# Kernel tuning notes

Hardware: AMD Instinct MI355X
Metric: run time of the kernel (lower is better)

The kernel has to match this reference:

```python
import jax, jax.numpy as jnp
import numpy as np

DIM = 1024
HEADS = 16
HEAD_DIM = DIM // HEADS
SCALE = HEAD_DIM ** -0.5


def setup_inputs() -> dict:
    key = jax.random.key(0)
    ks = jax.random.split(key, 9)
    b, n, m = 4, 1024, 1024
    x = jax.random.normal(ks[0], (b, n, DIM), dtype=jnp.float32)
    context = jax.random.normal(ks[1], (b, m, DIM), dtype=jnp.float32)
    mask = jax.random.randint(ks[2], (b, n, 32, 32), 0, 2, dtype=jnp.int32)
    s = DIM ** -0.5
    Wq = jax.random.normal(ks[3], (DIM, DIM), dtype=jnp.float32) * s
    bq = jnp.zeros((DIM,), dtype=jnp.float32)
    Wkv = jax.random.normal(ks[4], (DIM, 2 * DIM), dtype=jnp.float32) * s
    bkv = jnp.zeros((2 * DIM,), dtype=jnp.float32)
    Wp = jax.random.normal(ks[5], (DIM, DIM), dtype=jnp.float32) * s
    bp = jnp.zeros((DIM,), dtype=jnp.float32)
    return {"x": x, "context": context, "mask": mask,
            "Wq": Wq, "bq": bq, "Wkv": Wkv, "bkv": bkv, "Wp": Wp, "bp": bp}


def reference(x, context, mask, Wq, bq, Wkv, bkv, Wp, bp):
    b, n, _ = x.shape
    m = context.shape[1]
    h, d = HEADS, HEAD_DIM
    # projections
    q = (x @ Wq + bq).reshape(b, n, h, d).transpose(0, 2, 1, 3)       # [b,h,n,d]
    kv = (context @ Wkv + bkv).reshape(b, m, 2, h, d)
    k = kv[:, :, 0].transpose(0, 2, 1, 3)                              # [b,h,m,d]
    v = kv[:, :, 1].transpose(0, 2, 1, 3)                              # [b,h,m,d]
    dots = jnp.einsum('bhnd,bhmd->bhnm', q, k) * SCALE                 # [b,h,n,m]
    # mask: [b,n,H,W] -> [b,1,n,m]; masked_fill where mask == 0
    mflat = mask.reshape(b, n, m)[:, None]                             # [b,1,n,m]
    dots = jnp.where(mflat == 0, -jnp.inf, dots)
    attn = jax.nn.softmax(dots, axis=-1)
    out = jnp.einsum('bhnm,bhmd->bhnd', attn, v)
    out = out.transpose(0, 2, 1, 3).reshape(b, n, h * d)
    return out @ Wp + bp
```

## Files before the change

### kernel.cpp

```cpp
#include <hip/hip_runtime.h>

typedef __bf16 bf16;
typedef __bf16 bf16x8 __attribute__((ext_vector_type(8)));
typedef float f32x4 __attribute__((ext_vector_type(4)));
typedef unsigned long long u64;

#define MFMA16(a, b, c) __builtin_amdgcn_mfma_f32_16x16x32_bf16(a, b, c, 0, 0, 0)

__device__ __forceinline__ void gl_lds16(const void* g, void* l) {
  __builtin_amdgcn_global_load_lds(
      (const __attribute__((address_space(1))) unsigned int*)g,
      (__attribute__((address_space(3))) unsigned int*)l, 16, 0, 0);
}

__global__ __launch_bounds__(256)
void prep_k(const float* __restrict__ Wq, const float* __restrict__ Wkv,
            const float* __restrict__ Wp, const int* __restrict__ mask,
            const float* __restrict__ context, const float* __restrict__ x,
            bf16* __restrict__ BqkvT, bf16* __restrict__ WpT,
            u64* __restrict__ maskbits, bf16* __restrict__ cb,
            bf16* __restrict__ xb) {
  const int bx = blockIdx.x;
  const int tid = threadIdx.x;
  if (bx >= 3328) {
    const size_t i = ((size_t)(bx - 3328) * 256 + tid) * 8;
    f32x4 a0 = *(const f32x4*)(x + i);
    f32x4 a1 = *(const f32x4*)(x + i + 4);
    bf16x8 t;
#pragma unroll
    for (int j = 0; j < 4; ++j) { t[j] = (bf16)a0[j]; t[4 + j] = (bf16)a1[j]; }
    *(bf16x8*)(xb + i) = t;
    return;
  }
  if (bx >= 1280) {
    const size_t i = ((size_t)(bx - 1280) * 256 + tid) * 8;
    f32x4 a0 = *(const f32x4*)(context + i);
    f32x4 a1 = *(const f32x4*)(context + i + 4);
    bf16x8 t;
#pragma unroll
    for (int j = 0; j < 4; ++j) { t[j] = (bf16)a0[j]; t[4 + j] = (bf16)a1[j]; }
    *(bf16x8*)(cb + i) = t;
    return;
  }
  if (bx >= 1024) {
    const int idx = (bx - 1024) * 256 + tid;
    const int4* p = (const int4*)(mask + (size_t)idx * 64);
    u64 v = 0;
#pragma unroll
    for (int i = 0; i < 16; ++i) {
      int4 m = p[i];
      v |= (u64)(m.x != 0) << (4 * i);
      v |= (u64)(m.y != 0) << (4 * i + 1);
      v |= (u64)(m.z != 0) << (4 * i + 2);
      v |= (u64)(m.w != 0) << (4 * i + 3);
    }
    maskbits[idx] = v;
    return;
  }
  const int ct = bx >> 4, rt = bx & 15;
  const float* src;
  bf16* dst;
  int C, c0, drow0;
  if (ct < 16) {
    src = Wq; C = 1024; c0 = ct * 64; dst = BqkvT; drow0 = c0;
  } else if (ct < 48) {
    src = Wkv; C = 2048; c0 = (ct - 16) * 64; dst = BqkvT; drow0 = 1024 + c0;
  } else {
    src = Wp; C = 1024; c0 = (ct - 48) * 64; dst = WpT; drow0 = c0;
  }
  __shared__ bf16 T[64][72];
  const int r0 = rt * 64;
#pragma unroll
  for (int i = 0; i < 2; ++i) {
    int c = i * 256 + tid;
    int row = c >> 3, col = (c & 7) * 8;
    const float* sp = &src[(size_t)(r0 + row) * C + c0 + col];
    f32x4 a0 = *(const f32x4*)sp;
    f32x4 a1 = *(const f32x4*)(sp + 4);
    bf16x8 t;
#pragma unroll
    for (int j = 0; j < 4; ++j) { t[j] = (bf16)a0[j]; t[4 + j] = (bf16)a1[j]; }
    *(bf16x8*)&T[row][col] = t;
  }
  __syncthreads();
#pragma unroll
  for (int i = 0; i < 2; ++i) {
    int c = i * 256 + tid;
    int orow = c >> 3, ocol = (c & 7) * 8;
    bf16x8 v;
#pragma unroll
    for (int j = 0; j < 8; ++j) v[j] = T[ocol + j][orow];
    *(bf16x8*)&dst[(size_t)(drow0 + orow) * 1024 + r0 + ocol] = v;
  }
}

template <int EPI, int BN>
__global__ __launch_bounds__(256)
void gemm_sb(const bf16* __restrict__ A0, const bf16* __restrict__ A1,
             const bf16* __restrict__ Bt, const float* __restrict__ bias0,
             const float* __restrict__ bias1, bf16* __restrict__ oq,
             bf16* __restrict__ ok, bf16* __restrict__ ovt,
             float* __restrict__ outf) {
  constexpr int NJ = BN / 32;
  __shared__ bf16 As[128][64];
  __shared__ bf16 Bs[BN][64];
  const int tid = threadIdx.x;
  const int lane = tid & 63;
  const int w = tid >> 6;
  const int wm = (w >> 1) * 64;
  const int wn = (w & 1) * (BN / 2);
  const int l15 = lane & 15, l4 = lane >> 4;
  const int lrow = lane >> 3;
  const int scol = ((lane & 7) ^ (lrow & 7)) * 8;
  const int m0 = blockIdx.x * 128;
  const int n0 = blockIdx.y * BN;

  const bf16* Asrc = (EPI == 1) ? ((n0 < 1024) ? A0 : A1) : A0;

  f32x4 acc[4][NJ] = {};

  for (int k = 0; k < 16; ++k) {
    const int kk = k * 64;
#pragma unroll
    for (int it = 0; it < 4; ++it) {
      const int r = w * 32 + it * 8;
      gl_lds16(&Asrc[(size_t)(m0 + r + lrow) * 1024 + kk + scol], &As[r][0]);
    }
#pragma unroll
    for (int it = 0; it < BN / 32; ++it) {
      const int r = w * (BN / 4) + it * 8;
      gl_lds16(&Bt[(size_t)(n0 + r + lrow) * 1024 + kk + scol], &Bs[r][0]);
    }
    __syncthreads();
#pragma unroll
    for (int ks = 0; ks < 2; ++ks) {
      const int sw = ((ks * 4 + l4) ^ (l15 & 7)) * 8;
      bf16x8 af[4], bfr[NJ];
#pragma unroll
      for (int i = 0; i < 4; ++i)
        af[i] = *(const bf16x8*)&As[wm + i * 16 + l15][sw];
#pragma unroll
      for (int j = 0; j < NJ; ++j)
        bfr[j] = *(const bf16x8*)&Bs[wn + j * 16 + l15][sw];
#pragma unroll
      for (int i = 0; i < 4; ++i)
#pragma unroll
        for (int j = 0; j < NJ; ++j)
          acc[i][j] = MFMA16(af[i], bfr[j], acc[i][j]);
    }
    __syncthreads();
  }

  const float SCALE2 = 0.18033688011112042f;
#pragma unroll
  for (int j = 0; j < NJ; ++j) {
    const int col = n0 + wn + j * 16 + l15;
    float bc;
    if (EPI == 1) bc = (col < 1024) ? bias0[col] : bias1[col - 1024];
    else bc = bias0[col];
#pragma unroll
    for (int i = 0; i < 4; ++i) {
#pragma unroll
      for (int r = 0; r < 4; ++r) {
        const int row = m0 + wm + i * 16 + l4 * 4 + r;
        const float v = acc[i][j][r] + bc;
        if (EPI == 0) {
          outf[(size_t)row * 1024 + col] = v;
        } else {
          const int b = row >> 10, n = row & 1023;
          if (col < 1024) {
            const int h = col >> 6, d = col & 63;
            oq[(((size_t)(b * 16 + h)) * 1024 + n) * 64 + d] =
                (bf16)(v * SCALE2);
          } else {
            const int ckv = col - 1024;
            const int s = ckv >> 10, c2 = ckv & 1023;
            const int h = c2 >> 6, d = c2 & 63;
            if (s == 0)
              ok[(((size_t)(b * 16 + h)) * 1024 + n) * 64 + d] = (bf16)v;
            else
              ovt[(((size_t)(b * 16 + h)) * 64 + d) * 1024 + n] = (bf16)v;
          }
        }
      }
    }
  }
}

__global__ __launch_bounds__(256)
void attn_kernel(const bf16* __restrict__ q, const bf16* __restrict__ k,
                 const bf16* __restrict__ vT, const u64* __restrict__ maskbits,
                 bf16* __restrict__ ao) {
  const int bh = blockIdx.x;
  const int ntile = blockIdx.y;
  const int b = bh >> 4, h = bh & 15;
  const int tid = threadIdx.x;
  const int lane = tid & 63;
  const int w = tid >> 6;
  const int l15 = lane & 15, l4 = lane >> 4;

  __shared__ bf16 Ks[64][72];
  __shared__ bf16 Vts[64][72];
  __shared__ bf16 Pw[4][16][72];

  const size_t base = (size_t)bh * 65536;
  const int nrow0 = ntile * 64 + w * 16;

  bf16x8 qf[2];
#pragma unroll
  for (int ks = 0; ks < 2; ++ks)
    qf[ks] =
        *(const bf16x8*)&q[base + (size_t)(nrow0 + l15) * 64 + ks * 32 + l4 * 8];

  f32x4 o[4] = {};
  float lsum[4] = {0.0f, 0.0f, 0.0f, 0.0f};

  const u64* mb = maskbits + (size_t)(b * 1024 + nrow0) * 16;

  for (int mt = 0; mt < 16; ++mt) {
#pragma unroll
    for (int i = 0; i < 2; ++i) {
      int c = i * 256 + tid;
      int row = c >> 3, col = (c & 7) * 8;
      *(bf16x8*)&Ks[row][col] =
          *(const bf16x8*)&k[base + (size_t)(mt * 64 + row) * 64 + col];
      *(bf16x8*)&Vts[row][col] =
          *(const bf16x8*)&vT[base + (size_t)row * 1024 + mt * 64 + col];
    }
    __syncthreads();

    f32x4 s[4];
#pragma unroll
    for (int sub = 0; sub < 4; ++sub) s[sub] = f32x4{-12.f, -12.f, -12.f, -12.f};
#pragma unroll
    for (int ks = 0; ks < 2; ++ks) {
#pragma unroll
      for (int sub = 0; sub < 4; ++sub) {
        bf16x8 bfr = *(const bf16x8*)&Ks[sub * 16 + l15][ks * 32 + l4 * 8];
        s[sub] = MFMA16(qf[ks], bfr, s[sub]);
      }
    }

    u64 wbits[4];
#pragma unroll
    for (int r = 0; r < 4; ++r) wbits[r] = mb[(size_t)(l4 * 4 + r) * 16 + mt];

#pragma unroll
    for (int sub = 0; sub < 4; ++sub) {
#pragma unroll
      for (int r = 0; r < 4; ++r) {
        float p = exp2f(s[sub][r]);
        p = ((wbits[r] >> (sub * 16 + l15)) & 1) ? p : 0.0f;
        lsum[r] += p;
        Pw[w][l4 * 4 + r][sub * 16 + l15] = (bf16)p;
      }
    }

#pragma unroll
    for (int ks = 0; ks < 2; ++ks) {
      bf16x8 af = *(const bf16x8*)&Pw[w][l15][ks * 32 + l4 * 8];
#pragma unroll
      for (int sub = 0; sub < 4; ++sub) {
        bf16x8 bfr = *(const bf16x8*)&Vts[sub * 16 + l15][ks * 32 + l4 * 8];
        o[sub] = MFMA16(af, bfr, o[sub]);
      }
    }
    __syncthreads();
  }

  float inv[4];
#pragma unroll
  for (int r = 0; r < 4; ++r) {
    float t = lsum[r];
#pragma unroll
    for (int d = 1; d < 16; d <<= 1) t += __shfl_xor(t, d);
    inv[r] = 1.0f / t;
  }

#pragma unroll
  for (int sub = 0; sub < 4; ++sub) {
#pragma unroll
    for (int r = 0; r < 4; ++r) {
      const int n = nrow0 + l4 * 4 + r;
      const size_t idx =
          ((size_t)(b * 1024 + n)) * 1024 + h * 64 + sub * 16 + l15;
      ao[idx] = (bf16)(o[sub][r] * inv[r]);
    }
  }
}

extern "C" void kernel_launch(void* const* d_in, const int* in_sizes, int n_in,
                              void* d_out, int out_size, void* d_ws,
                              size_t ws_size, hipStream_t stream) {
  const float* x = (const float*)d_in[0];
  const float* context = (const float*)d_in[1];
  const int* mask = (const int*)d_in[2];
  const float* Wq = (const float*)d_in[3];
  const float* bq = (const float*)d_in[4];
  const float* Wkv = (const float*)d_in[5];
  const float* bkv = (const float*)d_in[6];
  const float* Wp = (const float*)d_in[7];
  const float* bp = (const float*)d_in[8];
  float* out = (float*)d_out;

  char* ws = (char*)d_ws;
  bf16* cb = (bf16*)(ws);
  bf16* aow = (bf16*)(ws);
  bf16* xb = (bf16*)(ws + (8ull << 20));
  bf16* BqkvT = (bf16*)(ws + (16ull << 20));
  bf16* qw = (bf16*)(ws + (22ull << 20));
  bf16* kw = (bf16*)(ws + (30ull << 20));
  bf16* vtw = (bf16*)(ws + (38ull << 20));
  u64* maskbits = (u64*)(ws + (46ull << 20));
  bf16* WpT = (bf16*)(ws + (46ull << 20) + (512ull << 10));

  const dim3 blk(256);

  prep_k<<<dim3(5376), blk, 0, stream>>>(Wq, Wkv, Wp, mask, context, x, BqkvT,
                                         WpT, maskbits, cb, xb);

  gemm_sb<1, 128><<<dim3(32, 24), blk, 0, stream>>>(xb, cb, BqkvT, bq, bkv,
                                                    qw, kw, vtw, nullptr);

  attn_kernel<<<dim3(64, 16), blk, 0, stream>>>(qw, kw, vtw, maskbits, aow);

  gemm_sb<0, 64><<<dim3(32, 16), blk, 0, stream>>>(aow, nullptr, WpT, bp,
                                                   nullptr, nullptr, nullptr,
                                                   nullptr, out);
}
```

Baseline: 219.2 us.

## Double-buffer GEMM LDS tiles with K=32 stages to overlap loads and MFMA

Both projection GEMMs switch from a single-buffered 64-wide K tile to double-buffered 32-wide K tiles. The next tile's async global-to-LDS load is issued before computing the current one. The LDS swizzle is reworked for the narrower rows, and launch bounds now request 3 blocks per CU. This aims to hide global load latency behind MFMA work, at the cost of more barriers per K step and a smaller compute chunk between syncs.

New measurement: 219.7 us. Within noise of the previous version (+0.2%).

```diff
diff --git a/kernel.cpp b/kernel.cpp
--- a/kernel.cpp
+++ b/kernel.cpp
@@ -95,23 +95,24 @@
 }
 
 template <int EPI, int BN>
-__global__ __launch_bounds__(256)
-void gemm_sb(const bf16* __restrict__ A0, const bf16* __restrict__ A1,
-             const bf16* __restrict__ Bt, const float* __restrict__ bias0,
-             const float* __restrict__ bias1, bf16* __restrict__ oq,
-             bf16* __restrict__ ok, bf16* __restrict__ ovt,
-             float* __restrict__ outf) {
+__global__ __launch_bounds__(256, 3)
+void gemm_db2(const bf16* __restrict__ A0, const bf16* __restrict__ A1,
+              const bf16* __restrict__ Bt, const float* __restrict__ bias0,
+              const float* __restrict__ bias1, bf16* __restrict__ oq,
+              bf16* __restrict__ ok, bf16* __restrict__ ovt,
+              float* __restrict__ outf) {
   constexpr int NJ = BN / 32;
-  __shared__ bf16 As[128][64];
-  __shared__ bf16 Bs[BN][64];
+  __shared__ bf16 As[2][128][32];
+  __shared__ bf16 Bs[2][BN][32];
   const int tid = threadIdx.x;
   const int lane = tid & 63;
   const int w = tid >> 6;
   const int wm = (w >> 1) * 64;
   const int wn = (w & 1) * (BN / 2);
   const int l15 = lane & 15, l4 = lane >> 4;
-  const int lrow = lane >> 3;
-  const int scol = ((lane & 7) ^ (lrow & 7)) * 8;
+  const int lrow = lane >> 2;
+  const int lcg = (lane & 3) ^ ((lrow >> 1) & 3);
+  const int rdc = (l4 ^ ((l15 >> 1) & 3)) * 8;
   const int m0 = blockIdx.x * 128;
   const int n0 = blockIdx.y * BN;
 
@@ -119,37 +120,43 @@
 
   f32x4 acc[4][NJ] = {};
 
-  for (int k = 0; k < 16; ++k) {
-    const int kk = k * 64;
-#pragma unroll
-    for (int it = 0; it < 4; ++it) {
-      const int r = w * 32 + it * 8;
-      gl_lds16(&Asrc[(size_t)(m0 + r + lrow) * 1024 + kk + scol], &As[r][0]);
-    }
-#pragma unroll
-    for (int it = 0; it < BN / 32; ++it) {
-      const int r = w * (BN / 4) + it * 8;
-      gl_lds16(&Bt[(size_t)(n0 + r + lrow) * 1024 + kk + scol], &Bs[r][0]);
-    }
+#define STAGE(kk, buf)                                                        \
+  {                                                                           \
+    _Pragma("unroll") for (int it = 0; it < 2; ++it) {                        \
+      const int r = w * 32 + it * 16;                                         \
+      gl_lds16(&Asrc[(size_t)(m0 + r + lrow) * 1024 + (kk) + lcg * 8],        \
+               &As[buf][r][0]);                                               \
+    }                                                                         \
+    _Pragma("unroll") for (int it = 0; it < BN / 64; ++it) {                  \
+      const int r = w * (BN / 4) + it * 16;                                   \
+      gl_lds16(&Bt[(size_t)(n0 + r + lrow) * 1024 + (kk) + lcg * 8],          \
+               &Bs[buf][r][0]);                                               \
+    }                                                                         \
+  }
+
+#define COMPUTE(buf)                                                          \
+  {                                                                           \
+    bf16x8 af[4], bfr[NJ];                                                    \
+    _Pragma("unroll") for (int i = 0; i < 4; ++i) af[i] =                     \
+        *(const bf16x8*)&As[buf][wm + i * 16 + l15][rdc];                     \
+    _Pragma("unroll") for (int j = 0; j < NJ; ++j) bfr[j] =                   \
+        *(const bf16x8*)&Bs[buf][wn + j * 16 + l15][rdc];                     \
+    _Pragma("unroll") for (int i = 0; i < 4; ++i)                             \
+        _Pragma("unroll") for (int j = 0; j < NJ; ++j) acc[i][j] =            \
+            MFMA16(af[i], bfr[j], acc[i][j]);                                 \
+  }
+
+  STAGE(0, 0);
+  for (int k = 0; k < 32; k += 2) {
     __syncthreads();
-#pragma unroll
-    for (int ks = 0; ks < 2; ++ks) {
-      const int sw = ((ks * 4 + l4) ^ (l15 & 7)) * 8;
-      bf16x8 af[4], bfr[NJ];
-#pragma unroll
-      for (int i = 0; i < 4; ++i)
-        af[i] = *(const bf16x8*)&As[wm + i * 16 + l15][sw];
-#pragma unroll
-      for (int j = 0; j < NJ; ++j)
-        bfr[j] = *(const bf16x8*)&Bs[wn + j * 16 + l15][sw];
-#pragma unroll
-      for (int i = 0; i < 4; ++i)
-#pragma unroll
-        for (int j = 0; j < NJ; ++j)
-          acc[i][j] = MFMA16(af[i], bfr[j], acc[i][j]);
-    }
+    STAGE((k + 1) * 32, 1);
+    COMPUTE(0);
     __syncthreads();
-  }
+    if (k < 30) STAGE((k + 2) * 32, 0);
+    COMPUTE(1);
+  }
+#undef STAGE
+#undef COMPUTE
 
   const float SCALE2 = 0.18033688011112042f;
 #pragma unroll
@@ -319,12 +326,12 @@
   prep_k<<<dim3(5376), blk, 0, stream>>>(Wq, Wkv, Wp, mask, context, x, BqkvT,
                                          WpT, maskbits, cb, xb);
 
-  gemm_sb<1, 128><<<dim3(32, 24), blk, 0, stream>>>(xb, cb, BqkvT, bq, bkv,
-                                                    qw, kw, vtw, nullptr);
+  gemm_db2<1, 128><<<dim3(32, 24), blk, 0, stream>>>(xb, cb, BqkvT, bq, bkv,
+                                                     qw, kw, vtw, nullptr);
 
   attn_kernel<<<dim3(64, 16), blk, 0, stream>>>(qw, kw, vtw, maskbits, aow);
 
-  gemm_sb<0, 64><<<dim3(32, 16), blk, 0, stream>>>(aow, nullptr, WpT, bp,
-                                                   nullptr, nullptr, nullptr,
-                                                   nullptr, out);
-}
+  gemm_db2<0, 64><<<dim3(32, 16), blk, 0, stream>>>(aow, nullptr, WpT, bp,
+                                                    nullptr, nullptr, nullptr,
+                                                    nullptr, out);
+}
```
